# Kernel tuning notes

Hardware: AMD Instinct MI355X
Metric: run time of the kernel (lower is better)

The kernel has to match this reference:

```python
import jax, jax.numpy as jnp
import numpy as np

B, S, I, W, H = 32, 2048, 32, 20, 128  # batch, seq_len, input_size, window_size, hidden_size
LN_EPS = 1e-5


def setup_inputs() -> dict:
    key = jax.random.key(0)
    ks = jax.random.split(key, 12)
    sc = lambda fan: 1.0 / np.sqrt(fan)
    x = jax.random.normal(ks[0], (B, S, I), jnp.float32)
    # encoder: Linear(W*I -> H) + LayerNorm(H) (+ GELU, dropout inactive at eval)
    W_enc = jax.random.normal(ks[1], (W * I, H), jnp.float32) * sc(W * I)
    b_enc = jnp.zeros((H,), jnp.float32)
    gamma = jnp.ones((H,), jnp.float32)
    beta = jnp.zeros((H,), jnp.float32)
    # comparator: Linear(2H->H), GELU, Linear(H->H//2), GELU, Linear(H//2->1), Sigmoid
    W1 = jax.random.normal(ks[2], (2 * H, H), jnp.float32) * sc(2 * H)
    b1 = jnp.zeros((H,), jnp.float32)
    W2 = jax.random.normal(ks[3], (H, H // 2), jnp.float32) * sc(H)
    b2 = jnp.zeros((H // 2,), jnp.float32)
    W3 = jax.random.normal(ks[4], (H // 2, 1), jnp.float32) * sc(H // 2)
    b3 = jnp.zeros((1,), jnp.float32)
    return dict(x=x, W_enc=W_enc, b_enc=b_enc, gamma=gamma, beta=beta,
                W1=W1, b1=b1, W2=W2, b2=b2, W3=W3, b3=b3)


def _gelu(v):
    return jax.nn.gelu(v, approximate=False)  # torch nn.GELU default is exact erf


def reference(x, W_enc, b_enc, gamma, beta, W1, b1, W2, b2, W3, b3):
    Bs, Ss, Is = x.shape
    Wd = W_enc.shape[0] // Is  # window_size
    nwin = Ss - Wd + 1
    # gather all sliding windows once: (B, nwin, Wd*I)
    idx = jnp.arange(nwin)[:, None] + jnp.arange(Wd)[None, :]
    win = x[:, idx, :].reshape(Bs, nwin, Wd * Is)
    # encoder: one big GEMM over all windows (before(t) == window at t-Wd, after(t) == window at t)
    h = win @ W_enc + b_enc
    mu = jnp.mean(h, axis=-1, keepdims=True)
    var = jnp.mean((h - mu) ** 2, axis=-1, keepdims=True)
    enc = _gelu((h - mu) / jnp.sqrt(var + LN_EPS) * gamma + beta)  # (B, nwin, H)
    T = Ss - 2 * Wd  # number of valid changepoint positions t in [Wd, Ss-Wd)
    combined = jnp.concatenate([enc[:, :T], enc[:, Wd:Wd + T]], axis=-1)  # (B, T, 2H)
    z = _gelu(combined @ W1 + b1)
    z = _gelu(z @ W2 + b2)
    p = jax.nn.sigmoid((z @ W3 + b3)[..., 0])  # (B, T)
    probs = jnp.pad(p, ((0, 0), (Wd, Wd)))  # zero pad to (B, S)
    return probs, probs > 0.5
```

## Files before the change

### kernel.cpp

```cpp
#include <hip/hip_runtime.h>
#include <hip/hip_bf16.h>
#include <math.h>

namespace {

constexpr int kB = 32;
constexpr int kS = 2048;
constexpr int kI = 32;
constexpr int kW = 20;
constexpr int kH = 128;
constexpr int kNwin = kS - kW + 1;
constexpr int kT = kS - 2 * kW;
constexpr float kEps = 1e-5f;
constexpr int FCAP = 16384;
constexpr float kMargin = 3e-3f;

typedef __attribute__((ext_vector_type(8))) _Float16 half8;
typedef __attribute__((ext_vector_type(8))) unsigned short ush8;
typedef __attribute__((ext_vector_type(4))) float f32x4;

#define GLD16(SRC, DST)                                                          \
    __builtin_amdgcn_global_load_lds(                                            \
        (const __attribute__((address_space(1))) unsigned*)(const void*)(SRC),   \
        (__attribute__((address_space(3))) unsigned*)(void*)(DST), 16, 0, 0)

__device__ __forceinline__ unsigned short f2h(float f) {
    _Float16 h = (_Float16)f;
    return __builtin_bit_cast(unsigned short, h);
}
__device__ __forceinline__ float gelu_exact(float v) {
    return 0.5f * v * (1.0f + erff(v * 0.70710678118654752440f));
}

constexpr size_t ENCB_OFF = 0;
constexpr size_t WEF_OFF  = 16777216;
constexpr size_t W1F_OFF  = WEF_OFF + 163840;
constexpr size_t W2F_OFF  = W1F_OFF + 65536;
constexpr size_t FC_OFF   = W2F_OFF + 16384;
constexpr size_t FL_OFF   = FC_OFF + 64;

__global__ void prep_kernel(const float* __restrict__ Wenc, const float* __restrict__ W1,
                            const float* __restrict__ W2,
                            unsigned short* __restrict__ WeF, unsigned short* __restrict__ W1F,
                            unsigned short* __restrict__ W2F)
{
    const int tid = blockIdx.x * blockDim.x + threadIdx.x;
    const int nth = gridDim.x * blockDim.x;
    for (int i = tid; i < 20 * 4 * 128 * 8; i += nth) {
        int j = i & 7, n = (i >> 3) & 127, rg = (i >> 10) & 3, kc = i >> 12;
        int k = kc * 32 + rg * 8 + j;
        WeF[i] = f2h(Wenc[(size_t)k * kH + n]);
    }
    for (int i = tid; i < 4 * 2 * 4 * 128 * 8; i += nth) {
        int j = i & 7, n = (i >> 3) & 127, rg = (i >> 10) & 3, ks = (i >> 12) & 1, kc = i >> 13;
        int k = kc * 64 + ks * 32 + rg * 8 + j;
        W1F[i] = f2h(W1[(size_t)k * kH + n]);
    }
    for (int i = tid; i < 2 * 2 * 4 * 64 * 8; i += nth) {
        int j = i & 7, n = (i >> 3) & 63, rg = (i >> 9) & 3, ks = (i >> 11) & 1, kc2 = i >> 12;
        int k = kc2 * 64 + ks * 32 + rg * 8 + j;
        W2F[i] = f2h(W2[(size_t)k * 64 + n]);
    }
}

constexpr int AP = 40;

__global__ __launch_bounds__(512, 4)
void enc_kernel(const float* __restrict__ x, const unsigned short* __restrict__ WeF,
                const float* __restrict__ benc, const float* __restrict__ gma,
                const float* __restrict__ bta, unsigned short* __restrict__ encb)
{
    __shared__ unsigned short xsh[147 * AP];
    __shared__ unsigned short wth[4096];
    __shared__ float red[2][128][2];

    const int tid = threadIdx.x, b = blockIdx.y, t0 = blockIdx.x * 128;
    const int l = tid & 63, w = tid >> 6;
    const int wr = w >> 1, wc = w & 1;
    const int cb = l & 15, rg = l >> 4;

    const float4* x4 = reinterpret_cast<const float4*>(x + (size_t)b * kS * kI);
    for (int i = tid; i < 147 * 8; i += 512) {
        int r = i >> 3, q = i & 7;
        int gr = t0 + r; if (gr > kS - 1) gr = kS - 1;
        float4 v = x4[gr * 8 + q];
        unsigned short h0 = f2h(v.x), h1 = f2h(v.y), h2 = f2h(v.z), h3 = f2h(v.w);
        *reinterpret_cast<uint2*>(&xsh[r * AP + q * 4]) =
            make_uint2((unsigned)h0 | ((unsigned)h1 << 16), (unsigned)h2 | ((unsigned)h3 << 16));
    }

    f32x4 acc[2][4];
    #pragma unroll
    for (int mi = 0; mi < 2; ++mi)
        #pragma unroll
        for (int nf = 0; nf < 4; ++nf) acc[mi][nf] = f32x4{0.f, 0.f, 0.f, 0.f};

    for (int kc = 0; kc < 20; ++kc) {
        __syncthreads();
        GLD16(WeF + (size_t)kc * 4096 + w * 512 + l * 8, &wth[w * 512]);
        __syncthreads();
        const int a0o = (wr * 32 + cb + kc) * AP + rg * 8;
        half8 a0 = *reinterpret_cast<const half8*>(&xsh[a0o]);
        half8 a1 = *reinterpret_cast<const half8*>(&xsh[a0o + 16 * AP]);
        #pragma unroll
        for (int nf = 0; nf < 4; ++nf) {
            const int bo = rg * 1024 + (wc * 64 + nf * 16 + cb) * 8;
            half8 bh = *reinterpret_cast<const half8*>(&wth[bo]);
            acc[0][nf] = __builtin_amdgcn_mfma_f32_16x16x32_f16(a0, bh, acc[0][nf], 0, 0, 0);
            acc[1][nf] = __builtin_amdgcn_mfma_f32_16x16x32_f16(a1, bh, acc[1][nf], 0, 0, 0);
        }
    }

    float bv[4], gv[4], btv[4];
    #pragma unroll
    for (int nf = 0; nf < 4; ++nf) {
        const int col = wc * 64 + nf * 16 + cb;
        bv[nf] = benc[col]; gv[nf] = gma[col]; btv[nf] = bta[col];
    }
    float h[2][4][4];
    #pragma unroll
    for (int mi = 0; mi < 2; ++mi)
        #pragma unroll
        for (int r = 0; r < 4; ++r) {
            float s = 0.f;
            #pragma unroll
            for (int nf = 0; nf < 4; ++nf) {
                h[mi][r][nf] = acc[mi][nf][r] + bv[nf];
                s += h[mi][r][nf];
            }
            s += __shfl_xor(s, 1); s += __shfl_xor(s, 2);
            s += __shfl_xor(s, 4); s += __shfl_xor(s, 8);
            if (cb == 0) red[0][wr * 32 + mi * 16 + rg * 4 + r][wc] = s;
        }
    __syncthreads();
    #pragma unroll
    for (int mi = 0; mi < 2; ++mi)
        #pragma unroll
        for (int r = 0; r < 4; ++r) {
            const int rl = wr * 32 + mi * 16 + rg * 4 + r;
            const float mu = (red[0][rl][0] + red[0][rl][1]) * (1.f / 128.f);
            float s2 = 0.f;
            #pragma unroll
            for (int nf = 0; nf < 4; ++nf) {
                h[mi][r][nf] -= mu;
                s2 += h[mi][r][nf] * h[mi][r][nf];
            }
            s2 += __shfl_xor(s2, 1); s2 += __shfl_xor(s2, 2);
            s2 += __shfl_xor(s2, 4); s2 += __shfl_xor(s2, 8);
            if (cb == 0) red[1][rl][wc] = s2;
        }
    __syncthreads();
    #pragma unroll
    for (int mi = 0; mi < 2; ++mi)
        #pragma unroll
        for (int r = 0; r < 4; ++r) {
            const int rl = wr * 32 + mi * 16 + rg * 4 + r;
            const int t = t0 + rl;
            const float var = (red[1][rl][0] + red[1][rl][1]) * (1.f / 128.f);
            const float rstd = 1.f / sqrtf(var + kEps);
            if (t < kNwin) {
                unsigned short* dst = encb + ((size_t)(b * kS + t)) * kH;
                #pragma unroll
                for (int nf = 0; nf < 4; ++nf) {
                    float v = gelu_exact(h[mi][r][nf] * rstd * gv[nf] + btv[nf]);
                    dst[wc * 64 + nf * 16 + cb] = f2h(v);
                }
            }
        }
}

constexpr int EPP = 72;

__global__ __launch_bounds__(512, 4)
void cmp_kernel(const unsigned short* __restrict__ encb,
                const unsigned short* __restrict__ W1F, const float* __restrict__ b1,
                const unsigned short* __restrict__ W2F, const float* __restrict__ b2,
                const float* __restrict__ W3, const float* __restrict__ b3,
                float* __restrict__ out, int* __restrict__ fcnt, unsigned* __restrict__ flist)
{
    __shared__ __align__(16) unsigned short pool[12800];
    __shared__ float prm[192];

    unsigned short* esh  = pool;
    unsigned short* wt1h = pool + 4608;

    const int tid = threadIdx.x, b = blockIdx.y, t0 = blockIdx.x * 64;
    const int l = tid & 63, w = tid >> 6;
    const int wr = w >> 1, wc = w & 1;
    const int cb = l & 15, rg = l >> 4;

    if (tid < 128) prm[tid] = b1[tid];
    else if (tid < 192) prm[tid] = b2[tid - 128];

    f32x4 acc1[4];
    #pragma unroll
    for (int nf = 0; nf < 4; ++nf) acc1[nf] = f32x4{0.f, 0.f, 0.f, 0.f};

    for (int kc = 0; kc < 4; ++kc) {
        const int ro = (kc < 2) ? 0 : kW, co = (kc & 1) * 64;
        __syncthreads();
        GLD16(W1F + (size_t)kc * 8192 + w * 512 + l * 8, &wt1h[w * 512]);
        GLD16(W1F + (size_t)kc * 8192 + 4096 + w * 512 + l * 8, &wt1h[4096 + w * 512]);
        {
            const int r = tid >> 3, qq = tid & 7;
            int gr = t0 + ro + r; if (gr > kNwin - 1) gr = kNwin - 1;
            *reinterpret_cast<ush8*>(&esh[r * EPP + qq * 8]) =
                *reinterpret_cast<const ush8*>(encb + ((size_t)(b * kS + gr)) * kH + co + qq * 8);
        }
        __syncthreads();
        #pragma unroll
        for (int ks = 0; ks < 2; ++ks) {
            const int ao = (wr * 16 + cb) * EPP + ks * 32 + rg * 8;
            half8 ah = *reinterpret_cast<const half8*>(&esh[ao]);
            #pragma unroll
            for (int nf = 0; nf < 4; ++nf) {
                const int bo = (ks * 4 + rg) * 1024 + (wc * 64 + nf * 16 + cb) * 8;
                half8 bh = *reinterpret_cast<const half8*>(&wt1h[bo]);
                acc1[nf] = __builtin_amdgcn_mfma_f32_16x16x32_f16(ah, bh, acc1[nf], 0, 0, 0);
            }
        }
    }
    __syncthreads();
    unsigned short* z1h = pool;
    unsigned short* w2h = pool + 8704;
    #pragma unroll
    for (int r = 0; r < 4; ++r) {
        const int row = wr * 16 + rg * 4 + r;
        #pragma unroll
        for (int nf = 0; nf < 4; ++nf) {
            const int col = wc * 64 + nf * 16 + cb;
            z1h[row * 136 + col] = f2h(gelu_exact(acc1[nf][r] + prm[col]));
        }
    }

    f32x4 acc2[2];
    #pragma unroll
    for (int nf = 0; nf < 2; ++nf) acc2[nf] = f32x4{0.f, 0.f, 0.f, 0.f};

    for (int kc2 = 0; kc2 < 2; ++kc2) {
        __syncthreads();
        GLD16(W2F + (size_t)kc2 * 4096 + w * 512 + l * 8, &w2h[w * 512]);
        __syncthreads();
        #pragma unroll
        for (int ks = 0; ks < 2; ++ks) {
            const int ao = (wr * 16 + cb) * 136 + kc2 * 64 + ks * 32 + rg * 8;
            half8 ah = *reinterpret_cast<const half8*>(&z1h[ao]);
            #pragma unroll
            for (int nf = 0; nf < 2; ++nf) {
                const int bo = (ks * 4 + rg) * 512 + (wc * 32 + nf * 16 + cb) * 8;
                half8 bh = *reinterpret_cast<const half8*>(&w2h[bo]);
                acc2[nf] = __builtin_amdgcn_mfma_f32_16x16x32_f16(ah, bh, acc2[nf], 0, 0, 0);
            }
        }
    }
    __syncthreads();
    float* z2f = reinterpret_cast<float*>(pool);
    #pragma unroll
    for (int r = 0; r < 4; ++r) {
        const int row = wr * 16 + rg * 4 + r;
        #pragma unroll
        for (int nf = 0; nf < 2; ++nf) {
            const int col = wc * 32 + nf * 16 + cb;
            z2f[row * 68 + col] = gelu_exact(acc2[nf][r] + prm[128 + col]);
        }
    }
    __syncthreads();

    if (tid < 64) {
        const int t = t0 + tid;
        if (t < kT) {
            float s = 0.f;
            #pragma unroll 8
            for (int k = 0; k < 64; ++k) s = fmaf(z2f[tid * 68 + k], W3[k], s);
            const float p = 1.f / (1.f + expf(-(s + b3[0])));
            out[(size_t)b * kS + t + kW] = p;
            out[(size_t)kB * kS + (size_t)b * kS + t + kW] = (p > 0.5f) ? 1.f : 0.f;
            if (fabsf(p - 0.5f) < kMargin) {
                int idx = atomicAdd(fcnt, 1);
                if (idx < FCAP) flist[idx] = ((unsigned)b << 16) | (unsigned)t;
            }
        }
    }
}

__global__ __launch_bounds__(256, 2)
void fix4_kernel(const float* __restrict__ x, const float* __restrict__ Wenc,
                 const float* __restrict__ benc, const float* __restrict__ gma,
                 const float* __restrict__ bta, const float* __restrict__ W1,
                 const float* __restrict__ b1, const float* __restrict__ W2,
                 const float* __restrict__ b2, const float* __restrict__ W3,
                 const float* __restrict__ b3, const int* __restrict__ fcnt,
                 const unsigned* __restrict__ flist, float* __restrict__ out)
{
    __shared__ float Wc[8192];
    __shared__ float xwc[1024];
    __shared__ float es[2048];
    __shared__ float z1s[1024];
    __shared__ float z2s[512];
    __shared__ unsigned pbt[8];

    const int tid = threadIdx.x;
    const int wv = tid >> 6, l = tid & 63;
    const int p = tid >> 5, cq = tid & 31;
    int n = *fcnt; if (n > FCAP) n = FCAP;
    if (n <= 0) return;
    const int nb = (n + 7) >> 3;

    for (int ib = blockIdx.x; ib < nb; ib += gridDim.x) {
        __syncthreads();
        if (tid < 8) {
            int idx = ib * 8 + tid; if (idx > n - 1) idx = n - 1;
            pbt[tid] = flist[idx];
        }
        __syncthreads();

        float acc[2][4];
        #pragma unroll
        for (int r = 0; r < 2; ++r)
            #pragma unroll
            for (int j = 0; j < 4; ++j) acc[r][j] = 0.f;

        for (int kc = 0; kc < 10; ++kc) {
            __syncthreads();
            {
                const float* src = Wenc + (size_t)kc * 8192;
                #pragma unroll
                for (int q = 0; q < 8; ++q)
                    GLD16(src + (wv * 8 + q) * 256 + l * 4, &Wc[(wv * 8 + q) * 256]);
            }
            {
                const int kq = tid & 15, pp = (tid >> 4) & 7, r = tid >> 7;
                const unsigned e = pbt[pp];
                const int bb = (int)(e >> 16), tt = (int)(e & 0xFFFF);
                const float4 v = *reinterpret_cast<const float4*>(
                    x + ((size_t)bb * kS + tt + r * kW) * kI + kc * 64 + kq * 4);
                *reinterpret_cast<float4*>(&xwc[(r * 8 + pp) * 64 + kq * 4]) = v;
            }
            __syncthreads();
            #pragma unroll 4
            for (int kk = 0; kk < 64; ++kk) {
                const float a0 = xwc[p * 64 + kk];
                const float a1 = xwc[(8 + p) * 64 + kk];
                const float4 wv4 = *reinterpret_cast<const float4*>(&Wc[kk * 128 + cq * 4]);
                acc[0][0] = fmaf(a0, wv4.x, acc[0][0]);
                acc[0][1] = fmaf(a0, wv4.y, acc[0][1]);
                acc[0][2] = fmaf(a0, wv4.z, acc[0][2]);
                acc[0][3] = fmaf(a0, wv4.w, acc[0][3]);
                acc[1][0] = fmaf(a1, wv4.x, acc[1][0]);
                acc[1][1] = fmaf(a1, wv4.y, acc[1][1]);
                acc[1][2] = fmaf(a1, wv4.z, acc[1][2]);
                acc[1][3] = fmaf(a1, wv4.w, acc[1][3]);
            }
        }

        const float4 bv = *reinterpret_cast<const float4*>(benc + cq * 4);
        const float4 gv = *reinterpret_cast<const float4*>(gma + cq * 4);
        const float4 bt = *reinterpret_cast<const float4*>(bta + cq * 4);
        #pragma unroll
        for (int r = 0; r < 2; ++r) {
            float hv[4];
            hv[0] = acc[r][0] + bv.x; hv[1] = acc[r][1] + bv.y;
            hv[2] = acc[r][2] + bv.z; hv[3] = acc[r][3] + bv.w;
            float s = hv[0] + hv[1] + hv[2] + hv[3];
            s += __shfl_xor(s, 1); s += __shfl_xor(s, 2); s += __shfl_xor(s, 4);
            s += __shfl_xor(s, 8); s += __shfl_xor(s, 16);
            const float mu = s * (1.f / 128.f);
            float s2 = 0.f;
            #pragma unroll
            for (int j = 0; j < 4; ++j) { hv[j] -= mu; s2 += hv[j] * hv[j]; }
            s2 += __shfl_xor(s2, 1); s2 += __shfl_xor(s2, 2); s2 += __shfl_xor(s2, 4);
            s2 += __shfl_xor(s2, 8); s2 += __shfl_xor(s2, 16);
            const float rstd = 1.f / sqrtf(s2 * (1.f / 128.f) + kEps);
            float o[4];
            o[0] = gelu_exact(hv[0] * rstd * gv.x + bt.x);
            o[1] = gelu_exact(hv[1] * rstd * gv.y + bt.y);
            o[2] = gelu_exact(hv[2] * rstd * gv.z + bt.z);
            o[3] = gelu_exact(hv[3] * rstd * gv.w + bt.w);
            *reinterpret_cast<float4*>(&es[p * 256 + r * 128 + cq * 4]) =
                make_float4(o[0], o[1], o[2], o[3]);
        }

        {
            float z[4] = {0.f, 0.f, 0.f, 0.f};
            for (int kc1 = 0; kc1 < 4; ++kc1) {
                __syncthreads();
                const float* src = W1 + (size_t)kc1 * 8192;
                #pragma unroll
                for (int q = 0; q < 8; ++q)
                    GLD16(src + (wv * 8 + q) * 256 + l * 4, &Wc[(wv * 8 + q) * 256]);
                __syncthreads();
                #pragma unroll 4
                for (int kk = 0; kk < 64; ++kk) {
                    const float a = es[p * 256 + kc1 * 64 + kk];
                    const float4 wv4 = *reinterpret_cast<const float4*>(&Wc[kk * 128 + cq * 4]);
                    z[0] = fmaf(a, wv4.x, z[0]);
                    z[1] = fmaf(a, wv4.y, z[1]);
                    z[2] = fmaf(a, wv4.z, z[2]);
                    z[3] = fmaf(a, wv4.w, z[3]);
                }
            }
            const float4 b1v = *reinterpret_cast<const float4*>(b1 + cq * 4);
            *reinterpret_cast<float4*>(&z1s[p * 128 + cq * 4]) = make_float4(
                gelu_exact(z[0] + b1v.x), gelu_exact(z[1] + b1v.y),
                gelu_exact(z[2] + b1v.z), gelu_exact(z[3] + b1v.w));
        }

        __syncthreads();
        {
            #pragma unroll
            for (int q = 0; q < 8; ++q)
                GLD16(W2 + (wv * 8 + q) * 256 + l * 4, &Wc[(wv * 8 + q) * 256]);
        }
        __syncthreads();
        if (cq < 16) {
            float z[4] = {0.f, 0.f, 0.f, 0.f};
            #pragma unroll 4
            for (int kk = 0; kk < 128; ++kk) {
                const float a = z1s[p * 128 + kk];
                const float4 wv4 = *reinterpret_cast<const float4*>(&Wc[kk * 64 + cq * 4]);
                z[0] = fmaf(a, wv4.x, z[0]);
                z[1] = fmaf(a, wv4.y, z[1]);
                z[2] = fmaf(a, wv4.z, z[2]);
                z[3] = fmaf(a, wv4.w, z[3]);
            }
            const float4 b2v = *reinterpret_cast<const float4*>(b2 + cq * 4);
            *reinterpret_cast<float4*>(&z2s[p * 64 + cq * 4]) = make_float4(
                gelu_exact(z[0] + b2v.x), gelu_exact(z[1] + b2v.y),
                gelu_exact(z[2] + b2v.z), gelu_exact(z[3] + b2v.w));
        }
        __syncthreads();

        {
            float s = z2s[p * 64 + cq] * W3[cq] + z2s[p * 64 + cq + 32] * W3[cq + 32];
            s += __shfl_xor(s, 1); s += __shfl_xor(s, 2); s += __shfl_xor(s, 4);
            s += __shfl_xor(s, 8); s += __shfl_xor(s, 16);
            if (cq == 0) {
                const unsigned e = pbt[p];
                const int bb = (int)(e >> 16), tt = (int)(e & 0xFFFF);
                const float pr = 1.f / (1.f + expf(-(s + b3[0])));
                out[(size_t)bb * kS + tt + kW] = pr;
                out[(size_t)kB * kS + (size_t)bb * kS + tt + kW] = (pr > 0.5f) ? 1.f : 0.f;
            }
        }
    }
}

}

extern "C" void kernel_launch(void* const* d_in, const int* in_sizes, int n_in,
                              void* d_out, int out_size, void* d_ws, size_t ws_size,
                              hipStream_t stream)
{
    const float* x    = (const float*)d_in[0];
    const float* Wenc = (const float*)d_in[1];
    const float* benc = (const float*)d_in[2];
    const float* gma  = (const float*)d_in[3];
    const float* bta  = (const float*)d_in[4];
    const float* W1   = (const float*)d_in[5];
    const float* b1   = (const float*)d_in[6];
    const float* W2   = (const float*)d_in[7];
    const float* b2   = (const float*)d_in[8];
    const float* W3   = (const float*)d_in[9];
    const float* b3   = (const float*)d_in[10];
    float* out = (float*)d_out;

    char* ws = (char*)d_ws;
    unsigned short* encb  = (unsigned short*)(ws + ENCB_OFF);
    unsigned short* WeF   = (unsigned short*)(ws + WEF_OFF);
    unsigned short* W1F   = (unsigned short*)(ws + W1F_OFF);
    unsigned short* W2F   = (unsigned short*)(ws + W2F_OFF);
    int* fcnt             = (int*)(ws + FC_OFF);
    unsigned* flist       = (unsigned*)(ws + FL_OFF);

    hipMemsetAsync(d_out, 0, (size_t)out_size * sizeof(float), stream);
    hipMemsetAsync(fcnt, 0, 64, stream);

    prep_kernel<<<256, 256, 0, stream>>>(Wenc, W1, W2, WeF, W1F, W2F);
    enc_kernel<<<dim3(16, kB), 512, 0, stream>>>(x, WeF, benc, gma, bta, encb);
    cmp_kernel<<<dim3(32, kB), 512, 0, stream>>>(encb, W1F, b1, W2F, b2, W3, b3,
                                                 out, fcnt, flist);
    fix4_kernel<<<512, 256, 0, stream>>>(x, Wenc, benc, gma, bta, W1, b1, W2, b2, W3, b3,
                                         fcnt, flist, out);
}
```

Baseline: 112.6 us.

## Double-buffer weight and input chunks in the fp32 fixup kernel

```diff
diff --git a/kernel.cpp b/kernel.cpp
--- a/kernel.cpp
+++ b/kernel.cpp
@@ -284,7 +284,7 @@
 }
 
 __global__ __launch_bounds__(256, 2)
-void fix4_kernel(const float* __restrict__ x, const float* __restrict__ Wenc,
+void fix5_kernel(const float* __restrict__ x, const float* __restrict__ Wenc,
                  const float* __restrict__ benc, const float* __restrict__ gma,
                  const float* __restrict__ bta, const float* __restrict__ W1,
                  const float* __restrict__ b1, const float* __restrict__ W2,
@@ -292,20 +292,27 @@
                  const float* __restrict__ b3, const int* __restrict__ fcnt,
                  const unsigned* __restrict__ flist, float* __restrict__ out)
 {
-    __shared__ float Wc[8192];
-    __shared__ float xwc[1024];
-    __shared__ float es[2048];
-    __shared__ float z1s[1024];
-    __shared__ float z2s[512];
+    __shared__ float Wc[2][4096];
+    __shared__ float xwc[2][16][32];
+    __shared__ float es[8][256];
+    __shared__ float z1s[8][128];
+    __shared__ float z2s[8][64];
     __shared__ unsigned pbt[8];
 
     const int tid = threadIdx.x;
     const int wv = tid >> 6, l = tid & 63;
     const int p = tid >> 5, cq = tid & 31;
+    const int rp = tid >> 3, xq = tid & 7;
     int n = *fcnt; if (n > FCAP) n = FCAP;
     if (n <= 0) return;
     const int nb = (n + 7) >> 3;
 
+#define DMA_W32(SRC, BUF)                                                        \
+    {   const float* _s = (SRC);                                                 \
+        _Pragma("unroll")                                                        \
+        for (int q = 0; q < 4; ++q)                                              \
+            GLD16(_s + (wv * 4 + q) * 256 + l * 4, &Wc[BUF][(wv * 4 + q) * 256]); }
+
     for (int ib = blockIdx.x; ib < nb; ib += gridDim.x) {
         __syncthreads();
         if (tid < 8) {
@@ -314,34 +321,37 @@
         }
         __syncthreads();
 
+        int xbase = 0;
+        if (tid < 128) {
+            const int r = rp >> 3, pp = rp & 7;
+            const unsigned e = pbt[pp];
+            xbase = (((int)(e >> 16)) * kS + (int)(e & 0xFFFF) + r * kW) * kI;
+        }
+
         float acc[2][4];
         #pragma unroll
         for (int r = 0; r < 2; ++r)
             #pragma unroll
             for (int j = 0; j < 4; ++j) acc[r][j] = 0.f;
 
-        for (int kc = 0; kc < 10; ++kc) {
-            __syncthreads();
-            {
-                const float* src = Wenc + (size_t)kc * 8192;
-                #pragma unroll
-                for (int q = 0; q < 8; ++q)
-                    GLD16(src + (wv * 8 + q) * 256 + l * 4, &Wc[(wv * 8 + q) * 256]);
-            }
-            {
-                const int kq = tid & 15, pp = (tid >> 4) & 7, r = tid >> 7;
-                const unsigned e = pbt[pp];
-                const int bb = (int)(e >> 16), tt = (int)(e & 0xFFFF);
-                const float4 v = *reinterpret_cast<const float4*>(
-                    x + ((size_t)bb * kS + tt + r * kW) * kI + kc * 64 + kq * 4);
-                *reinterpret_cast<float4*>(&xwc[(r * 8 + pp) * 64 + kq * 4]) = v;
-            }
-            __syncthreads();
+        float4 xreg;
+        if (tid < 128) xreg = *reinterpret_cast<const float4*>(x + xbase + xq * 4);
+        DMA_W32(Wenc + 0, 0);
+        if (tid < 128) *reinterpret_cast<float4*>(&xwc[0][rp][xq * 4]) = xreg;
+        __syncthreads();
+
+        for (int kc = 0; kc < 20; ++kc) {
+            const int cur = kc & 1;
+            if (kc < 19) {
+                if (tid < 128)
+                    xreg = *reinterpret_cast<const float4*>(x + xbase + (kc + 1) * 32 + xq * 4);
+                DMA_W32(Wenc + (size_t)(kc + 1) * 4096, cur ^ 1);
+            }
             #pragma unroll 4
-            for (int kk = 0; kk < 64; ++kk) {
-                const float a0 = xwc[p * 64 + kk];
-                const float a1 = xwc[(8 + p) * 64 + kk];
-                const float4 wv4 = *reinterpret_cast<const float4*>(&Wc[kk * 128 + cq * 4]);
+            for (int kk = 0; kk < 32; ++kk) {
+                const float a0 = xwc[cur][p][kk];
+                const float a1 = xwc[cur][8 + p][kk];
+                const float4 wv4 = *reinterpret_cast<const float4*>(&Wc[cur][kk * 128 + cq * 4]);
                 acc[0][0] = fmaf(a0, wv4.x, acc[0][0]);
                 acc[0][1] = fmaf(a0, wv4.y, acc[0][1]);
                 acc[0][2] = fmaf(a0, wv4.z, acc[0][2]);
@@ -351,6 +361,9 @@
                 acc[1][2] = fmaf(a1, wv4.z, acc[1][2]);
                 acc[1][3] = fmaf(a1, wv4.w, acc[1][3]);
             }
+            if (kc < 19 && tid < 128)
+                *reinterpret_cast<float4*>(&xwc[cur ^ 1][rp][xq * 4]) = xreg;
+            __syncthreads();
         }
 
         const float4 bv = *reinterpret_cast<const float4*>(benc + cq * 4);
@@ -371,36 +384,34 @@
             s2 += __shfl_xor(s2, 1); s2 += __shfl_xor(s2, 2); s2 += __shfl_xor(s2, 4);
             s2 += __shfl_xor(s2, 8); s2 += __shfl_xor(s2, 16);
             const float rstd = 1.f / sqrtf(s2 * (1.f / 128.f) + kEps);
-            float o[4];
-            o[0] = gelu_exact(hv[0] * rstd * gv.x + bt.x);
-            o[1] = gelu_exact(hv[1] * rstd * gv.y + bt.y);
-            o[2] = gelu_exact(hv[2] * rstd * gv.z + bt.z);
-            o[3] = gelu_exact(hv[3] * rstd * gv.w + bt.w);
-            *reinterpret_cast<float4*>(&es[p * 256 + r * 128 + cq * 4]) =
-                make_float4(o[0], o[1], o[2], o[3]);
+            *reinterpret_cast<float4*>(&es[p][r * 128 + cq * 4]) = make_float4(
+                gelu_exact(hv[0] * rstd * gv.x + bt.x),
+                gelu_exact(hv[1] * rstd * gv.y + bt.y),
+                gelu_exact(hv[2] * rstd * gv.z + bt.z),
+                gelu_exact(hv[3] * rstd * gv.w + bt.w));
         }
 
         {
             float z[4] = {0.f, 0.f, 0.f, 0.f};
-            for (int kc1 = 0; kc1 < 4; ++kc1) {
-                __syncthreads();
-                const float* src = W1 + (size_t)kc1 * 8192;
-                #pragma unroll
-                for (int q = 0; q < 8; ++q)
-                    GLD16(src + (wv * 8 + q) * 256 + l * 4, &Wc[(wv * 8 + q) * 256]);
-                __syncthreads();
+            __syncthreads();
+            DMA_W32(W1 + 0, 0);
+            __syncthreads();
+            for (int kc1 = 0; kc1 < 8; ++kc1) {
+                const int cur = kc1 & 1;
+                if (kc1 < 7) DMA_W32(W1 + (size_t)(kc1 + 1) * 4096, cur ^ 1);
                 #pragma unroll 4
-                for (int kk = 0; kk < 64; ++kk) {
-                    const float a = es[p * 256 + kc1 * 64 + kk];
-                    const float4 wv4 = *reinterpret_cast<const float4*>(&Wc[kk * 128 + cq * 4]);
+                for (int kk = 0; kk < 32; ++kk) {
+                    const float a = es[p][kc1 * 32 + kk];
+                    const float4 wv4 = *reinterpret_cast<const float4*>(&Wc[cur][kk * 128 + cq * 4]);
                     z[0] = fmaf(a, wv4.x, z[0]);
                     z[1] = fmaf(a, wv4.y, z[1]);
                     z[2] = fmaf(a, wv4.z, z[2]);
                     z[3] = fmaf(a, wv4.w, z[3]);
                 }
+                __syncthreads();
             }
             const float4 b1v = *reinterpret_cast<const float4*>(b1 + cq * 4);
-            *reinterpret_cast<float4*>(&z1s[p * 128 + cq * 4]) = make_float4(
+            *reinterpret_cast<float4*>(&z1s[p][cq * 4]) = make_float4(
                 gelu_exact(z[0] + b1v.x), gelu_exact(z[1] + b1v.y),
                 gelu_exact(z[2] + b1v.z), gelu_exact(z[3] + b1v.w));
         }
@@ -408,30 +419,41 @@
         __syncthreads();
         {
             #pragma unroll
-            for (int q = 0; q < 8; ++q)
-                GLD16(W2 + (wv * 8 + q) * 256 + l * 4, &Wc[(wv * 8 + q) * 256]);
+            for (int q = 0; q < 4; ++q) {
+                GLD16(W2 + (wv * 4 + q) * 256 + l * 4, &Wc[0][(wv * 4 + q) * 256]);
+                GLD16(W2 + 4096 + (wv * 4 + q) * 256 + l * 4, &Wc[1][(wv * 4 + q) * 256]);
+            }
         }
         __syncthreads();
         if (cq < 16) {
             float z[4] = {0.f, 0.f, 0.f, 0.f};
             #pragma unroll 4
-            for (int kk = 0; kk < 128; ++kk) {
-                const float a = z1s[p * 128 + kk];
-                const float4 wv4 = *reinterpret_cast<const float4*>(&Wc[kk * 64 + cq * 4]);
+            for (int kk = 0; kk < 64; ++kk) {
+                const float a = z1s[p][kk];
+                const float4 wv4 = *reinterpret_cast<const float4*>(&Wc[0][kk * 64 + cq * 4]);
                 z[0] = fmaf(a, wv4.x, z[0]);
                 z[1] = fmaf(a, wv4.y, z[1]);
                 z[2] = fmaf(a, wv4.z, z[2]);
                 z[3] = fmaf(a, wv4.w, z[3]);
             }
+            #pragma unroll 4
+            for (int kk = 0; kk < 64; ++kk) {
+                const float a = z1s[p][64 + kk];
+                const float4 wv4 = *reinterpret_cast<const float4*>(&Wc[1][kk * 64 + cq * 4]);
+                z[0] = fmaf(a, wv4.x, z[0]);
+                z[1] = fmaf(a, wv4.y, z[1]);
+                z[2] = fmaf(a, wv4.z, z[2]);
+                z[3] = fmaf(a, wv4.w, z[3]);
+            }
             const float4 b2v = *reinterpret_cast<const float4*>(b2 + cq * 4);
-            *reinterpret_cast<float4*>(&z2s[p * 64 + cq * 4]) = make_float4(
+            *reinterpret_cast<float4*>(&z2s[p][cq * 4]) = make_float4(
                 gelu_exact(z[0] + b2v.x), gelu_exact(z[1] + b2v.y),
                 gelu_exact(z[2] + b2v.z), gelu_exact(z[3] + b2v.w));
         }
         __syncthreads();
 
         {
-            float s = z2s[p * 64 + cq] * W3[cq] + z2s[p * 64 + cq + 32] * W3[cq + 32];
+            float s = z2s[p][cq] * W3[cq] + z2s[p][cq + 32] * W3[cq + 32];
             s += __shfl_xor(s, 1); s += __shfl_xor(s, 2); s += __shfl_xor(s, 4);
             s += __shfl_xor(s, 8); s += __shfl_xor(s, 16);
             if (cq == 0) {
@@ -443,6 +465,7 @@
             }
         }
     }
+#undef DMA_W32
 }
 
 }
@@ -479,6 +502,6 @@
     enc_kernel<<<dim3(16, kB), 512, 0, stream>>>(x, WeF, benc, gma, bta, encb);
     cmp_kernel<<<dim3(32, kB), 512, 0, stream>>>(encb, W1F, b1, W2F, b2, W3, b3,
                                                  out, fcnt, flist);
-    fix4_kernel<<<512, 256, 0, stream>>>(x, Wenc, benc, gma, bta, W1, b1, W2, b2, W3, b3,
+    fix5_kernel<<<512, 256, 0, stream>>>(x, Wenc, benc, gma, bta, W1, b1, W2, b2, W3, b3,
                                          fcnt, flist, out);
 }
```

Result: slower. 117.2 us (+4.1%).
